# Optimization experiments

Hardware: AMD Instinct MI355X
Metric: run time of the kernel (lower is better)

Reference implementation:

```python
import jax, jax.numpy as jnp
import numpy as np
import math

J = 32            # output capsules (init j)
N = 16            # capsule dim (init n)
MASK_PERCENT = [0.4, 0.4]  # sparse top-k fractions per routing update


def squash(s, eps=1e-8):
    # v = (|s|^2 / (1+|s|^2)) * s/|s|
    sq = jnp.sum(s * s, axis=-1, keepdims=True)
    return (sq / (1.0 + sq)) * (s / jnp.sqrt(sq + eps))


def calc_entropy(c, axis):
    # -sum c*log(c), with 0*log0 := 0 (masked-out capsules have c == 0)
    safe = jnp.where(c > 0, c, 1.0)
    return -jnp.sum(jnp.where(c > 0, c * jnp.log(safe), 0.0), axis=axis)


def _sparsify_topk(b_vec, it, i):
    # method='topk', target='nodes': keep top select_count output capsules per example
    select_count = J
    for prev in MASK_PERCENT[: it + 1]:
        select_count = math.ceil(select_count * (1 - prev))
    if select_count >= J:
        return b_vec
    c = jax.nn.softmax(b_vec, axis=1)            # (b, j, i)
    scores = c.sum(axis=2) / i                   # (b, j) node scores
    _, idx = jax.lax.top_k(scores, select_count) # (b, k)
    b = scores.shape[0]
    sel = jnp.zeros((b, J), bool).at[jnp.arange(b)[:, None], idx].set(True)
    return jnp.where(sel[:, :, None], b_vec, -jnp.inf)


def setup_inputs() -> dict:
    key = jax.random.key(0)
    b, i = 128, 1152
    u_hat = jax.random.normal(key, (b, J, i, N), dtype=jnp.float32)
    bias = jnp.full((J, N), 0.1, dtype=jnp.float32)  # b_routing init 0.1
    return {"u_hat": u_hat, "bias": bias, "iters": 3}


def reference(u_hat, bias, iters):
    b, j, i, n = u_hat.shape
    b_vec = jnp.zeros((b, j, i), u_hat.dtype)
    entropies = []
    v_vec = None
    for index in range(iters):
        c_vec = jax.nn.softmax(b_vec, axis=1)                  # softmax over j
        entropies.append(calc_entropy(c_vec, axis=1).mean(axis=1))  # (b,)
        s_vec = jnp.einsum('bji,bjin->bjn', c_vec, u_hat)      # (b, j, n)
        reset_mask = jnp.sum(s_vec, axis=2) == 0               # (b, j)
        s_vec_bias = jnp.where(reset_mask[..., None], 0.0, s_vec + bias)
        v_vec = squash(s_vec_bias)                             # (b, j, n)
        if index < iters - 1:
            b_vec = b_vec + jnp.einsum('bjin,bjn->bji', u_hat, v_vec)
            b_vec = _sparsify_topk(b_vec, index, i)
    entropy_layer = jnp.stack(entropies, axis=1)               # (b, iters)
    return v_vec, entropy_layer
```

## Files before the change

### kernel.cpp

```cpp
#include <hip/hip_runtime.h>
#include <math.h>

#define B_ 128
#define J_ 32
#define I_ 1152
#define N_ 16
#define TI 16
#define STEPS 4
#define NT (I_/(TI*STEPS))

#define OFF_W   0
#define OFF_S1  65536
#define OFF_S2  131072
#define OFF_SC0 262144
#define OFF_SC1 266240
#define OFF_M0  270336
#define OFF_M1  274432

__global__ void zero_kernel(float* __restrict__ ws, float* __restrict__ ent) {
    int idx = blockIdx.x * 256 + threadIdx.x;
    for (int k = idx; k < 2 * 65536; k += gridDim.x * 256) ws[OFF_S1 + k] = 0.f;
    if (idx < 2 * 4096) ws[OFF_SC0 + idx] = 0.f;
    if (idx < B_ * 3) ent[idx] = 0.f;
}

__global__ void sumv_kernel(const float* __restrict__ U, const float* __restrict__ bias,
                            float* __restrict__ w, float* __restrict__ ent) {
    int bj  = blockIdx.x;
    int b = bj >> 5, j = bj & 31;
    int tid = threadIdx.x;
    int nc  = tid & 3;
    int ip  = tid >> 2;
    const float4* base = (const float4*)(U + (size_t)bj * I_ * N_);
    float4 acc = make_float4(0.f, 0.f, 0.f, 0.f);
    for (int i = ip; i < I_; i += 64) {
        float4 u = base[i * 4 + nc];
        acc.x += u.x; acc.y += u.y; acc.z += u.z; acc.w += u.w;
    }
    __shared__ float4 lds[256];
    lds[nc * 64 + ip] = acc;
    __syncthreads();
    for (int s = 32; s >= 1; s >>= 1) {
        if (ip < s) {
            float4 a = lds[nc * 64 + ip], c = lds[nc * 64 + ip + s];
            a.x += c.x; a.y += c.y; a.z += c.z; a.w += c.w;
            lds[nc * 64 + ip] = a;
        }
        __syncthreads();
    }
    if (tid < 16) {
        float sv = ((float*)&lds[(tid >> 2) * 64])[tid & 3] * (1.f / 32.f);
        float rs = sv;
        for (int k = 8; k; k >>= 1) rs += __shfl_xor(rs, k);
        float sb = (rs == 0.f) ? 0.f : sv + bias[j * N_ + tid];
        float sq = sb * sb;
        for (int k = 8; k; k >>= 1) sq += __shfl_xor(sq, k);
        float v = (sq / (1.f + sq)) * (sb / sqrtf(sq + 1e-8f));
        w[(b * J_ + j) * N_ + tid] = v;
        if (tid == 0 && j == 0) ent[b * 3] = logf(32.f);
    }
}

__global__ void vupdate_kernel(const float* __restrict__ s, const float* __restrict__ bias,
                               float* __restrict__ w, float* __restrict__ out_v,
                               float* __restrict__ ent, float scale, int mode) {
    int b = blockIdx.x;
    int tid = threadIdx.x;
    int j = tid >> 4, n = tid & 15;
    int idx = (b * J_ + j) * N_ + n;
    float sv = s[idx] * scale;
    float rs = sv;
    for (int k = 8; k; k >>= 1) rs += __shfl_xor(rs, k);
    float sb = (rs == 0.f) ? 0.f : sv + bias[j * N_ + n];
    float sq = sb * sb;
    for (int k = 8; k; k >>= 1) sq += __shfl_xor(sq, k);
    float v = (sq / (1.f + sq)) * (sb / sqrtf(sq + 1e-8f));
    if (mode == 1) {
        w[idx] += v;
    } else {
        out_v[idx] = v;
    }
}

__global__ __launch_bounds__(256) void pass_kernel(
        const float* __restrict__ U, const float* __restrict__ w,
        const int* __restrict__ mask, float* __restrict__ scores,
        float* __restrict__ s_out, float* __restrict__ ent,
        int ent_idx, int mode) {
    __shared__ float4 lds[J_ * (TI * 4 + 1)];
    __shared__ float le[256];
    __shared__ int jlist[32];
    __shared__ int posj[32];
    __shared__ int nact_s;

    int bid = blockIdx.x;
    int b = bid / NT, chunk = bid % NT;
    int i0 = chunk * (TI * STEPS);
    int tid = threadIdx.x;
    int j = tid & 31, sub = tid >> 5;

    if (tid < 32) {
        int act = mask ? (mask[b * J_ + tid] != 0) : 1;
        unsigned long long bal = __ballot(act);
        unsigned m32 = (unsigned)bal;
        int p = __popc(m32 & ((1u << tid) - 1));
        if (act) jlist[p] = tid;
        posj[tid] = act ? p : -1;
        if (tid == 0) nact_s = __popc(m32);
    }
    __syncthreads();
    int nact = nact_s;
    int pj = posj[j];
    bool active = pj >= 0;
    int pjc = active ? pj : 0;

    const float4* wp = (const float4*)(w + (b * J_ + j) * N_);
    float4 w0 = wp[0], w1 = wp[1], w2 = wp[2], w3 = wp[3];

    float acc_sc = 0.f, acc_ent = 0.f;
    float4 a0 = make_float4(0,0,0,0), a1 = a0, a2 = a0, a3 = a0;

    const float4* Ub = (const float4*)U;
    int tot = nact * 64;

    for (int st = 0; st < STEPS; ++st) {
        int ibase = i0 + st * TI;
        for (int f = tid; f < tot; f += 256) {
            int jc = f >> 6;
            int q  = f & 63;
            lds[jc * 65 + q] = Ub[((size_t)(b * J_ + jlist[jc]) * I_ + ibase) * 4 + q];
        }
        __syncthreads();
        #pragma unroll
        for (int t2 = 0; t2 < 2; ++t2) {
            int ii = sub + t2 * 8;
            const float4* up = &lds[pjc * 65 + ii * 4];
            float4 u0 = up[0], u1 = up[1], u2 = up[2], u3 = up[3];
            float y = u0.x * w0.x + u0.y * w0.y + u0.z * w0.z + u0.w * w0.w
                    + u1.x * w1.x + u1.y * w1.y + u1.z * w1.z + u1.w * w1.w
                    + u2.x * w2.x + u2.y * w2.y + u2.z * w2.z + u2.w * w2.w
                    + u3.x * w3.x + u3.y * w3.y + u3.z * w3.z + u3.w * w3.w;
            float e = active ? __expf(y) : 0.f;
            float Z = e;
            for (int k = 16; k; k >>= 1) Z += __shfl_xor(Z, k);
            float p = e / Z;
            if (mode == 0) {
                acc_sc += p;
            } else {
                a0.x += p * u0.x; a0.y += p * u0.y; a0.z += p * u0.z; a0.w += p * u0.w;
                a1.x += p * u1.x; a1.y += p * u1.y; a1.z += p * u1.z; a1.w += p * u1.w;
                a2.x += p * u2.x; a2.y += p * u2.y; a2.z += p * u2.z; a2.w += p * u2.w;
                a3.x += p * u3.x; a3.y += p * u3.y; a3.z += p * u3.z; a3.w += p * u3.w;
                acc_ent += p * (y - __logf(Z));
            }
        }
        __syncthreads();
    }

    if (mode == 0) {
        le[tid] = acc_sc;
        __syncthreads();
        if (tid < 32) {
            float t = 0.f;
            for (int s = 0; s < 8; s++) t += le[s * 32 + tid];
            atomicAdd(&scores[b * J_ + tid], t);
        }
    } else {
        float* ls = (float*)lds;
        float* myl = ls + tid * 16;
        ((float4*)myl)[0] = a0; ((float4*)myl)[1] = a1;
        ((float4*)myl)[2] = a2; ((float4*)myl)[3] = a3;
        le[tid] = acc_ent;
        __syncthreads();
        for (int idx = tid; idx < 512; idx += 256) {
            int jj = idx >> 4, nn = idx & 15;
            float t = 0.f;
            for (int s = 0; s < 8; s++) t += ls[(s * 32 + jj) * 16 + nn];
            atomicAdd(&s_out[(b * J_ + jj) * N_ + nn], t);
        }
        for (int s = 128; s >= 1; s >>= 1) {
            if (tid < s) le[tid] += le[tid + s];
            __syncthreads();
        }
        if (tid == 0) atomicAdd(&ent[b * 3 + ent_idx], -le[0] * (1.f / (float)I_));
    }
}

__global__ void topk_kernel(const float* __restrict__ scores, int* __restrict__ mask, int K) {
    int b = blockIdx.x;
    int tid = threadIdx.x;
    __shared__ float ls[32];
    if (tid < 32) ls[tid] = scores[b * 32 + tid];
    __syncthreads();
    if (tid < 32) {
        float sv = ls[tid];
        int rank = 0;
        for (int jj = 0; jj < 32; jj++) {
            float o = ls[jj];
            rank += (o > sv) || (o == sv && jj < tid);
        }
        mask[b * 32 + tid] = (rank < K) ? 1 : 0;
    }
}

extern "C" void kernel_launch(void* const* d_in, const int* in_sizes, int n_in,
                              void* d_out, int out_size, void* d_ws, size_t ws_size,
                              hipStream_t stream) {
    const float* U    = (const float*)d_in[0];
    const float* bias = (const float*)d_in[1];
    float* ws  = (float*)d_ws;
    float* out = (float*)d_out;
    float* ent = out + B_ * J_ * N_;

    float* w   = ws + OFF_W;
    float* s1  = ws + OFF_S1;
    float* s2  = ws + OFF_S2;
    float* sc0 = ws + OFF_SC0;
    float* sc1 = ws + OFF_SC1;
    int*   m0  = (int*)(ws + OFF_M0);
    int*   m1  = (int*)(ws + OFF_M1);

    zero_kernel<<<544, 256, 0, stream>>>(ws, ent);

    sumv_kernel<<<B_ * J_, 256, 0, stream>>>(U, bias, w, ent);

    pass_kernel<<<B_ * NT, 256, 0, stream>>>(U, w, nullptr, sc0, nullptr, nullptr, 0, 0);
    topk_kernel<<<B_, 64, 0, stream>>>(sc0, m0, 20);

    pass_kernel<<<B_ * NT, 256, 0, stream>>>(U, w, m0, nullptr, s1, ent, 1, 1);
    vupdate_kernel<<<B_, 512, 0, stream>>>(s1, bias, w, nullptr, ent, 1.f, 1);

    pass_kernel<<<B_ * NT, 256, 0, stream>>>(U, w, m0, sc1, nullptr, nullptr, 0, 0);
    topk_kernel<<<B_, 64, 0, stream>>>(sc1, m1, 12);

    pass_kernel<<<B_ * NT, 256, 0, stream>>>(U, w, m1, nullptr, s2, ent, 2, 1);
    vupdate_kernel<<<B_, 512, 0, stream>>>(s2, bias, nullptr, out, ent, 1.f, 2);
}
```

Before: 604.0 us.

## Fuse topk and squash epilogues into pass kernel via last-block tickets

Removes the separate zero, topk and vupdate kernels. Zeroing moves into sumv_kernel, and the per-batch top-k or squash update now runs in the last block of each batch inside pass_kernel, chosen with an atomic ticket counter plus thread fences. This cuts the launch count from ten to five and removes the small serial kernels between the passes. In exchange it adds fence and atomic overhead to every block, and correctness now depends on the ticket and fence ordering.

```diff
diff --git a/kernel.cpp b/kernel.cpp
--- a/kernel.cpp
+++ b/kernel.cpp
@@ -16,19 +16,25 @@
 #define OFF_SC1 266240
 #define OFF_M0  270336
 #define OFF_M1  274432
-
-__global__ void zero_kernel(float* __restrict__ ws, float* __restrict__ ent) {
-    int idx = blockIdx.x * 256 + threadIdx.x;
-    for (int k = idx; k < 2 * 65536; k += gridDim.x * 256) ws[OFF_S1 + k] = 0.f;
-    if (idx < 2 * 4096) ws[OFF_SC0 + idx] = 0.f;
-    if (idx < B_ * 3) ent[idx] = 0.f;
-}
-
-__global__ void sumv_kernel(const float* __restrict__ U, const float* __restrict__ bias,
-                            float* __restrict__ w, float* __restrict__ ent) {
+#define OFF_TK  278528
+
+__global__ __launch_bounds__(256) void sumv_kernel(const float* __restrict__ U,
+        const float* __restrict__ bias, float* __restrict__ ws,
+        float* __restrict__ ent) {
     int bj  = blockIdx.x;
     int b = bj >> 5, j = bj & 31;
     int tid = threadIdx.x;
+    int gb = bj * 256 + tid;
+
+    if (gb < 2 * 65536) ws[OFF_S1 + gb] = 0.f;
+    if (gb < 2 * 4096)  ws[OFF_SC0 + gb] = 0.f;
+    if (gb < 4 * B_)    ((int*)(ws + OFF_TK))[gb] = 0;
+    if (gb < B_) {
+        ent[gb * 3]     = logf(32.f);
+        ent[gb * 3 + 1] = 0.f;
+        ent[gb * 3 + 2] = 0.f;
+    }
+
     int nc  = tid & 3;
     int ip  = tid >> 2;
     const float4* base = (const float4*)(U + (size_t)bj * I_ * N_);
@@ -56,42 +62,23 @@
         float sq = sb * sb;
         for (int k = 8; k; k >>= 1) sq += __shfl_xor(sq, k);
         float v = (sq / (1.f + sq)) * (sb / sqrtf(sq + 1e-8f));
-        w[(b * J_ + j) * N_ + tid] = v;
-        if (tid == 0 && j == 0) ent[b * 3] = logf(32.f);
+        (ws + OFF_W)[(b * J_ + j) * N_ + tid] = v;
     }
 }
 
-__global__ void vupdate_kernel(const float* __restrict__ s, const float* __restrict__ bias,
-                               float* __restrict__ w, float* __restrict__ out_v,
-                               float* __restrict__ ent, float scale, int mode) {
-    int b = blockIdx.x;
-    int tid = threadIdx.x;
-    int j = tid >> 4, n = tid & 15;
-    int idx = (b * J_ + j) * N_ + n;
-    float sv = s[idx] * scale;
-    float rs = sv;
-    for (int k = 8; k; k >>= 1) rs += __shfl_xor(rs, k);
-    float sb = (rs == 0.f) ? 0.f : sv + bias[j * N_ + n];
-    float sq = sb * sb;
-    for (int k = 8; k; k >>= 1) sq += __shfl_xor(sq, k);
-    float v = (sq / (1.f + sq)) * (sb / sqrtf(sq + 1e-8f));
-    if (mode == 1) {
-        w[idx] += v;
-    } else {
-        out_v[idx] = v;
-    }
-}
-
 __global__ __launch_bounds__(256) void pass_kernel(
-        const float* __restrict__ U, const float* __restrict__ w,
+        const float* __restrict__ U, float* __restrict__ w,
         const int* __restrict__ mask, float* __restrict__ scores,
         float* __restrict__ s_out, float* __restrict__ ent,
-        int ent_idx, int mode) {
+        int ent_idx, int mode, int* __restrict__ ticket,
+        int* __restrict__ out_mask, int K,
+        const float* __restrict__ bias, float* __restrict__ out_v, int fin) {
     __shared__ float4 lds[J_ * (TI * 4 + 1)];
     __shared__ float le[256];
     __shared__ int jlist[32];
     __shared__ int posj[32];
     __shared__ int nact_s;
+    __shared__ int amlast;
 
     int bid = blockIdx.x;
     int b = bid / NT, chunk = bid % NT;
@@ -126,8 +113,7 @@
     for (int st = 0; st < STEPS; ++st) {
         int ibase = i0 + st * TI;
         for (int f = tid; f < tot; f += 256) {
-            int jc = f >> 6;
-            int q  = f & 63;
+            int jc = f >> 6, q = f & 63;
             lds[jc * 65 + q] = Ub[((size_t)(b * J_ + jlist[jc]) * I_ + ibase) * 4 + q];
         }
         __syncthreads();
@@ -184,22 +170,44 @@
         }
         if (tid == 0) atomicAdd(&ent[b * 3 + ent_idx], -le[0] * (1.f / (float)I_));
     }
-}
-
-__global__ void topk_kernel(const float* __restrict__ scores, int* __restrict__ mask, int K) {
-    int b = blockIdx.x;
-    int tid = threadIdx.x;
-    __shared__ float ls[32];
-    if (tid < 32) ls[tid] = scores[b * 32 + tid];
-    __syncthreads();
-    if (tid < 32) {
-        float sv = ls[tid];
-        int rank = 0;
-        for (int jj = 0; jj < 32; jj++) {
-            float o = ls[jj];
-            rank += (o > sv) || (o == sv && jj < tid);
-        }
-        mask[b * 32 + tid] = (rank < K) ? 1 : 0;
+
+    __syncthreads();
+    if (tid == 0) {
+        __threadfence();
+        int t = atomicAdd(&ticket[b], 1);
+        amlast = (t == NT - 1) ? 1 : 0;
+    }
+    __syncthreads();
+    if (!amlast) return;
+    __threadfence();
+
+    if (fin == 0) {
+        if (tid < 32) le[tid] = atomicAdd(&scores[b * 32 + tid], 0.f);
+        __syncthreads();
+        if (tid < 32) {
+            float sv = le[tid];
+            int rank = 0;
+            for (int jj = 0; jj < 32; jj++) {
+                float o = le[jj];
+                rank += (o > sv) || (o == sv && jj < tid);
+            }
+            out_mask[b * 32 + tid] = (rank < K) ? 1 : 0;
+        }
+    } else {
+        #pragma unroll
+        for (int half = 0; half < 2; ++half) {
+            int jj = half * 16 + (tid >> 4), n = tid & 15;
+            int idx = (b * J_ + jj) * N_ + n;
+            float sv = atomicAdd(&s_out[idx], 0.f);
+            float rs = sv;
+            for (int k = 8; k; k >>= 1) rs += __shfl_xor(rs, k);
+            float sb = (rs == 0.f) ? 0.f : sv + bias[jj * N_ + n];
+            float sq = sb * sb;
+            for (int k = 8; k; k >>= 1) sq += __shfl_xor(sq, k);
+            float v = (sq / (1.f + sq)) * (sb / sqrtf(sq + 1e-8f));
+            if (fin == 1) w[idx] += v;
+            else         out_v[idx] = v;
+        }
     }
 }
 
@@ -219,20 +227,19 @@
     float* sc1 = ws + OFF_SC1;
     int*   m0  = (int*)(ws + OFF_M0);
     int*   m1  = (int*)(ws + OFF_M1);
-
-    zero_kernel<<<544, 256, 0, stream>>>(ws, ent);
-
-    sumv_kernel<<<B_ * J_, 256, 0, stream>>>(U, bias, w, ent);
-
-    pass_kernel<<<B_ * NT, 256, 0, stream>>>(U, w, nullptr, sc0, nullptr, nullptr, 0, 0);
-    topk_kernel<<<B_, 64, 0, stream>>>(sc0, m0, 20);
-
-    pass_kernel<<<B_ * NT, 256, 0, stream>>>(U, w, m0, nullptr, s1, ent, 1, 1);
-    vupdate_kernel<<<B_, 512, 0, stream>>>(s1, bias, w, nullptr, ent, 1.f, 1);
-
-    pass_kernel<<<B_ * NT, 256, 0, stream>>>(U, w, m0, sc1, nullptr, nullptr, 0, 0);
-    topk_kernel<<<B_, 64, 0, stream>>>(sc1, m1, 12);
-
-    pass_kernel<<<B_ * NT, 256, 0, stream>>>(U, w, m1, nullptr, s2, ent, 2, 1);
-    vupdate_kernel<<<B_, 512, 0, stream>>>(s2, bias, nullptr, out, ent, 1.f, 2);
+    int*   tk  = (int*)(ws + OFF_TK);
+
+    sumv_kernel<<<B_ * J_, 256, 0, stream>>>(U, bias, ws, ent);
+
+    pass_kernel<<<B_ * NT, 256, 0, stream>>>(U, w, nullptr, sc0, nullptr, ent, 0, 0,
+                                             tk + 0 * B_, m0, 20, bias, nullptr, 0);
+
+    pass_kernel<<<B_ * NT, 256, 0, stream>>>(U, w, m0, nullptr, s1, ent, 1, 1,
+                                             tk + 1 * B_, nullptr, 0, bias, nullptr, 1);
+
+    pass_kernel<<<B_ * NT, 256, 0, stream>>>(U, w, m0, sc1, nullptr, ent, 0, 0,
+                                             tk + 2 * B_, m1, 12, bias, nullptr, 0);
+
+    pass_kernel<<<B_ * NT, 256, 0, stream>>>(U, w, m1, nullptr, s2, ent, 2, 1,
+                                             tk + 3 * B_, nullptr, 0, bias, out, 2);
 }
```

Measured after the change: 1.168 ms. +93.4%, slower.
